# Optimization experiments

Hardware: AMD Instinct MI355X
Metric: run time of the kernel (lower is better)

Reference implementation:

```python
import jax, jax.numpy as jnp
import numpy as np

N = 262144          # number of query points
NUM_AXES = 4        # input_dim + 2
RES = 512           # axis_resolution
EMB = 256           # embedding_dim
OUT = 3             # output_dim
W0 = 30.0           # Sine frequency


def setup_inputs() -> dict:
    key = jax.random.key(0)
    k_c, k_t, k_w1, k_b1, k_w2, k_b2 = jax.random.split(key, 6)
    coords = jax.random.uniform(k_c, (N, 2), jnp.float32, minval=-1.0, maxval=1.0)
    tables = jax.random.normal(k_t, (NUM_AXES, RES, EMB), jnp.float32) * 0.1
    # decoder: Linear(256,256) with first_layer_sine_init, Sine(30), Linear(256,3) with frequency_init(30)
    W1 = jax.random.uniform(k_w1, (256, EMB), jnp.float32, minval=-1.0 / EMB, maxval=1.0 / EMB)
    b1 = jax.random.uniform(k_b1, (256,), jnp.float32, minval=-0.0625, maxval=0.0625)
    lim2 = np.sqrt(6.0 / 256.0) / W0
    W2 = jax.random.uniform(k_w2, (OUT, 256), jnp.float32, minval=-lim2, maxval=lim2)
    b2 = jax.random.uniform(k_b2, (OUT,), jnp.float32, minval=-0.0625, maxval=0.0625)
    return {"coords": coords, "tables": tables, "W1": W1, "b1": b1, "W2": W2, "b2": b2}


def reference(coords, tables, W1, b1, W2, b2):
    # clamp input coords to [-1,1], build the 4 axis coordinates
    c = jnp.clip(coords, -1.0, 1.0)
    c = jnp.concatenate(
        [c, (c[:, 0:1] + c[:, 1:2]) * 0.5, (c[:, 0:1] - c[:, 1:2]) * 0.5], axis=-1
    )  # [N, 4]
    # linearInterpolate (vectorized over all axes at once)
    c = jnp.clip(c, -1.0, 0.999)
    t = (0.5 * c + 0.5) * (tables.shape[1] - 1)       # [N, 4] continuous index
    i0 = jnp.floor(t).astype(jnp.int32)               # [N, 4]
    w = (t - i0)[..., None]                           # [N, 4, 1]
    ax = jnp.arange(tables.shape[0])[None, :]         # [1, 4]
    v0 = tables[ax, i0]                               # [N, 4, EMB] gather
    v1 = tables[ax, i0 + 1]                           # [N, 4, EMB] gather
    emb = jnp.mean((1.0 - w) * v0 + w * v1, axis=1)   # [N, EMB] mean over axes
    # decoder: Linear -> Sine(30) -> Linear
    h = jnp.sin(W0 * (emb @ W1.T + b1))               # [N, 256]
    return h @ W2.T + b2                              # [N, 3]
```

## Files before the change

### kernel.cpp

```cpp
#include <hip/hip_runtime.h>
#include <hip/hip_bf16.h>
#include <hip/hip_fp16.h>

#define NPTS 262144
#define EMB  256
#define RES  512
#define NROWS (4 * RES)

typedef _Float16 half_t;
typedef __attribute__((ext_vector_type(8))) _Float16 half8;

__global__ __launch_bounds__(256) void t2_precompute_kernel(
    const float* __restrict__ tables,
    const float* __restrict__ W1,
    half_t* __restrict__ T2)
{
    __shared__ __align__(16) float arow[8][EMB];
    const int row0 = blockIdx.x * 8;
    const int o = threadIdx.x;

    #pragma unroll
    for (int r = 0; r < 8; ++r)
        arow[r][o] = tables[(row0 + r) * EMB + o];
    __syncthreads();

    float acc[8] = {0.f, 0.f, 0.f, 0.f, 0.f, 0.f, 0.f, 0.f};
    const float4* __restrict__ w1v = reinterpret_cast<const float4*>(W1 + o * EMB);
    for (int ec = 0; ec < EMB / 4; ++ec) {
        const float4 w4 = w1v[ec];
        #pragma unroll
        for (int r = 0; r < 8; ++r) {
            const float4 a4 = *reinterpret_cast<const float4*>(&arow[r][ec * 4]);
            acc[r] = fmaf(w4.x, a4.x, acc[r]);
            acc[r] = fmaf(w4.y, a4.y, acc[r]);
            acc[r] = fmaf(w4.z, a4.z, acc[r]);
            acc[r] = fmaf(w4.w, a4.w, acc[r]);
        }
    }
    const float s = 7.5f * 0.15915494309189535f;
    #pragma unroll
    for (int r = 0; r < 8; ++r)
        T2[(row0 + r) * EMB + o] = (half_t)(s * acc[r]);
}

__global__ __launch_bounds__(256, 8) void eval_kernel(
    const float* __restrict__ coords,
    const half_t* __restrict__ T2,
    const float* __restrict__ b1,
    const float* __restrict__ W2,
    const float* __restrict__ b2,
    float* __restrict__ out)
{
    const int lane = threadIdx.x & 63;
    const int hf   = lane >> 5;
    const int l    = lane & 31;
    const int e0   = l * 8;

    const int wave   = blockIdx.x * 4 + (threadIdx.x >> 6);
    const int nwaves = gridDim.x * 4;

    const float sb = 30.f * 0.15915494309189535f;
    float bias[8];
    float w2r[3][8];
    #pragma unroll
    for (int d = 0; d < 8; ++d) bias[d] = sb * b1[e0 + d];
    #pragma unroll
    for (int j = 0; j < 3; ++j)
        #pragma unroll
        for (int d = 0; d < 8; ++d) w2r[j][d] = W2[j * EMB + e0 + d];
    const float ob0 = b2[0], ob1 = b2[1], ob2 = b2[2];

    const char* __restrict__ T2b = reinterpret_cast<const char*>(T2);

    for (int pp = wave; pp < NPTS / 2; pp += nwaves) {
        const int p = 2 * pp + hf;
        const float2 cf = *reinterpret_cast<const float2*>(coords + 2 * p);
        const float x = fminf(fmaxf(cf.x, -1.f), 1.f);
        const float y = fminf(fmaxf(cf.y, -1.f), 1.f);

        float acc[8];
        #pragma unroll
        for (int d = 0; d < 8; ++d) acc[d] = bias[d];

        #pragma unroll
        for (int a = 0; a < 4; ++a) {
            float c = (a == 0) ? x : (a == 1) ? y
                    : (a == 2) ? 0.5f * (x + y) : 0.5f * (x - y);
            c = fminf(fmaxf(c, -1.f), 0.999f);
            const float t  = fmaf(c, 255.5f, 255.5f);
            const float fi = floorf(t);
            const float w  = t - fi;
            const float omw = 1.f - w;
            const int rowbyte = (((a << 9) + (int)fi) << 9) + (e0 << 1);
            const half8 v0 = *reinterpret_cast<const half8*>(T2b + rowbyte);
            const half8 v1 = *reinterpret_cast<const half8*>(T2b + rowbyte + 512);
            #pragma unroll
            for (int d = 0; d < 8; ++d) {
                acc[d] = fmaf((float)v0[d], omw, acc[d]);
                acc[d] = fmaf((float)v1[d], w,   acc[d]);
            }
        }

        float q0 = 0.f, q1 = 0.f, q2 = 0.f;
        #pragma unroll
        for (int d = 0; d < 8; ++d) {
            const float h = __builtin_amdgcn_sinf(__builtin_amdgcn_fractf(acc[d]));
            q0 = fmaf(h, w2r[0][d], q0);
            q1 = fmaf(h, w2r[1][d], q1);
            q2 = fmaf(h, w2r[2][d], q2);
        }

        #pragma unroll
        for (int off = 16; off > 0; off >>= 1) {
            q0 += __shfl_xor(q0, off, 64);
            q1 += __shfl_xor(q1, off, 64);
            q2 += __shfl_xor(q2, off, 64);
        }

        if (l == 0) {
            out[3 * p + 0] = q0 + ob0;
            out[3 * p + 1] = q1 + ob1;
            out[3 * p + 2] = q2 + ob2;
        }
    }
}

extern "C" void kernel_launch(void* const* d_in, const int* in_sizes, int n_in,
                              void* d_out, int out_size, void* d_ws, size_t ws_size,
                              hipStream_t stream) {
    const float* coords = (const float*)d_in[0];
    const float* tables = (const float*)d_in[1];
    const float* W1     = (const float*)d_in[2];
    const float* b1     = (const float*)d_in[3];
    const float* W2     = (const float*)d_in[4];
    const float* b2     = (const float*)d_in[5];
    float* out = (float*)d_out;

    half_t* T2 = (half_t*)d_ws;

    hipLaunchKernelGGL(t2_precompute_kernel, dim3(NROWS / 8), dim3(256), 0, stream,
                       tables, W1, T2);
    hipLaunchKernelGGL(eval_kernel, dim3(2048), dim3(256), 0, stream,
                       coords, T2, b1, W2, b2, out);
}
```

Before: 68.91 us.

## Use packed fp16 accumulation and 16-lane groups per point in eval kernel

Each wave now handles four points with 16 lanes per point and 16 embedding elements per lane, which shortens the shuffle reduction to four steps. The table interpolation is accumulated in packed half8 arithmetic, so the math can use packed fp16 FMAs instead of converting every element to float. W2 is held in fp16 registers and the occupancy hint in launch_bounds is dropped. The risks are lower precision in the fp16 accumulation of pre-sine arguments, which are scaled by 30/(2π), and higher register pressure.

```diff
diff --git a/kernel.cpp b/kernel.cpp
--- a/kernel.cpp
+++ b/kernel.cpp
@@ -43,7 +43,7 @@
         T2[(row0 + r) * EMB + o] = (half_t)(s * acc[r]);
 }
 
-__global__ __launch_bounds__(256, 8) void eval_kernel(
+__global__ __launch_bounds__(256) void eval_kernel(
     const float* __restrict__ coords,
     const half_t* __restrict__ T2,
     const float* __restrict__ b1,
@@ -52,35 +52,38 @@
     float* __restrict__ out)
 {
     const int lane = threadIdx.x & 63;
-    const int hf   = lane >> 5;
-    const int l    = lane & 31;
-    const int e0   = l * 8;
+    const int g    = lane >> 4;
+    const int l16  = lane & 15;
+    const int e0   = l16 * 16;
 
     const int wave   = blockIdx.x * 4 + (threadIdx.x >> 6);
     const int nwaves = gridDim.x * 4;
 
     const float sb = 30.f * 0.15915494309189535f;
-    float bias[8];
-    float w2r[3][8];
+    float bias[16];
     #pragma unroll
-    for (int d = 0; d < 8; ++d) bias[d] = sb * b1[e0 + d];
+    for (int d = 0; d < 16; ++d) bias[d] = sb * b1[e0 + d];
+
+    half8 w2h[3][2];
     #pragma unroll
     for (int j = 0; j < 3; ++j)
         #pragma unroll
-        for (int d = 0; d < 8; ++d) w2r[j][d] = W2[j * EMB + e0 + d];
+        for (int k = 0; k < 2; ++k)
+            #pragma unroll
+            for (int i = 0; i < 8; ++i)
+                w2h[j][k][i] = (half_t)W2[j * EMB + e0 + k * 8 + i];
+
     const float ob0 = b2[0], ob1 = b2[1], ob2 = b2[2];
-
     const char* __restrict__ T2b = reinterpret_cast<const char*>(T2);
 
-    for (int pp = wave; pp < NPTS / 2; pp += nwaves) {
-        const int p = 2 * pp + hf;
+    for (int pq = wave; pq < NPTS / 4; pq += nwaves) {
+        const int p = 4 * pq + g;
         const float2 cf = *reinterpret_cast<const float2*>(coords + 2 * p);
         const float x = fminf(fmaxf(cf.x, -1.f), 1.f);
         const float y = fminf(fmaxf(cf.y, -1.f), 1.f);
 
-        float acc[8];
-        #pragma unroll
-        for (int d = 0; d < 8; ++d) acc[d] = bias[d];
+        half8 accA = {0, 0, 0, 0, 0, 0, 0, 0};
+        half8 accB = {0, 0, 0, 0, 0, 0, 0, 0};
 
         #pragma unroll
         for (int a = 0; a < 4; ++a) {
@@ -90,34 +93,38 @@
             const float t  = fmaf(c, 255.5f, 255.5f);
             const float fi = floorf(t);
             const float w  = t - fi;
-            const float omw = 1.f - w;
-            const int rowbyte = (((a << 9) + (int)fi) << 9) + (e0 << 1);
-            const half8 v0 = *reinterpret_cast<const half8*>(T2b + rowbyte);
-            const half8 v1 = *reinterpret_cast<const half8*>(T2b + rowbyte + 512);
-            #pragma unroll
-            for (int d = 0; d < 8; ++d) {
-                acc[d] = fmaf((float)v0[d], omw, acc[d]);
-                acc[d] = fmaf((float)v1[d], w,   acc[d]);
-            }
+            const half_t hw   = (half_t)w;
+            const half_t homw = (half_t)(1.f - w);
+            const char* base = T2b + ((((a << 9) + (int)fi) << 9) + (e0 << 1));
+            const half8 v0a = *reinterpret_cast<const half8*>(base);
+            const half8 v0b = *reinterpret_cast<const half8*>(base + 16);
+            const half8 v1a = *reinterpret_cast<const half8*>(base + 512);
+            const half8 v1b = *reinterpret_cast<const half8*>(base + 528);
+            accA = v0a * homw + accA;
+            accA = v1a * hw   + accA;
+            accB = v0b * homw + accB;
+            accB = v1b * hw   + accB;
         }
 
         float q0 = 0.f, q1 = 0.f, q2 = 0.f;
         #pragma unroll
-        for (int d = 0; d < 8; ++d) {
-            const float h = __builtin_amdgcn_sinf(__builtin_amdgcn_fractf(acc[d]));
-            q0 = fmaf(h, w2r[0][d], q0);
-            q1 = fmaf(h, w2r[1][d], q1);
-            q2 = fmaf(h, w2r[2][d], q2);
+        for (int d = 0; d < 16; ++d) {
+            const half_t a16 = (d < 8) ? accA[d] : accB[d - 8];
+            const float arg = fmaf((float)a16, 1.0f, bias[d]);
+            const float h = __builtin_amdgcn_sinf(__builtin_amdgcn_fractf(arg));
+            q0 = fmaf(h, (float)w2h[0][d >> 3][d & 7], q0);
+            q1 = fmaf(h, (float)w2h[1][d >> 3][d & 7], q1);
+            q2 = fmaf(h, (float)w2h[2][d >> 3][d & 7], q2);
         }
 
         #pragma unroll
-        for (int off = 16; off > 0; off >>= 1) {
+        for (int off = 8; off > 0; off >>= 1) {
             q0 += __shfl_xor(q0, off, 64);
             q1 += __shfl_xor(q1, off, 64);
             q2 += __shfl_xor(q2, off, 64);
         }
 
-        if (l == 0) {
+        if (l16 == 0) {
             out[3 * p + 0] = q0 + ob0;
             out[3 * p + 1] = q1 + ob1;
             out[3 * p + 2] = q2 + ob2;
```

Result: faster. 66.36 us (-3.7%).

## Pipeline table gathers across points with packed fp16 interpolation and DPP reduction

Applied to the files above, without the earlier changes.

The eval kernel is restructured so each 16-lane group handles one point and covers 256 dims in two halves. The loop is fully unrolled over 8 points per wave, and the next point's gathers are prefetched while the current one is computed. Interpolation now runs in packed fp16 with half8 FMAs. The output projection uses fdot2, the fract before sin is dropped, and the shuffle reduction becomes a DPP reduction over 16 lanes. This is meant to hide gather latency and cut ALU work, at the cost of fp16 accumulation accuracy, more register pressure (launch bounds drop to 4), and a hardcoded grid-to-point mapping.

```diff
diff --git a/kernel.cpp b/kernel.cpp
--- a/kernel.cpp
+++ b/kernel.cpp
@@ -1,14 +1,13 @@
 #include <hip/hip_runtime.h>
-#include <hip/hip_bf16.h>
 #include <hip/hip_fp16.h>
 
 #define NPTS 262144
 #define EMB  256
-#define RES  512
-#define NROWS (4 * RES)
+#define NROWS 2048
 
 typedef _Float16 half_t;
 typedef __attribute__((ext_vector_type(8))) _Float16 half8;
+typedef __attribute__((ext_vector_type(2))) _Float16 half2v;
 
 __global__ __launch_bounds__(256) void t2_precompute_kernel(
     const float* __restrict__ tables,
@@ -43,7 +42,21 @@
         T2[(row0 + r) * EMB + o] = (half_t)(s * acc[r]);
 }
 
-__global__ __launch_bounds__(256, 8) void eval_kernel(
+template <int CTRL>
+__device__ __forceinline__ float dpp_add(float v) {
+    const int vi = __builtin_bit_cast(int, v);
+    const int sh = __builtin_amdgcn_update_dpp(0, vi, CTRL, 0xF, 0xF, true);
+    return v + __builtin_bit_cast(float, sh);
+}
+__device__ __forceinline__ float reduce16(float v) {
+    v = dpp_add<0xB1>(v);
+    v = dpp_add<0x4E>(v);
+    v = dpp_add<0x141>(v);
+    v = dpp_add<0x140>(v);
+    return v;
+}
+
+__global__ __launch_bounds__(256, 4) void eval_kernel(
     const float* __restrict__ coords,
     const half_t* __restrict__ T2,
     const float* __restrict__ b1,
@@ -52,76 +65,133 @@
     float* __restrict__ out)
 {
     const int lane = threadIdx.x & 63;
-    const int hf   = lane >> 5;
-    const int l    = lane & 31;
-    const int e0   = l * 8;
+    const int g    = lane >> 4;
+    const int l16  = lane & 15;
+    const int dA   = l16 * 8;
+    const int dB   = 128 + l16 * 8;
 
     const int wave   = blockIdx.x * 4 + (threadIdx.x >> 6);
-    const int nwaves = gridDim.x * 4;
+    const int stride = gridDim.x * 4;
 
     const float sb = 30.f * 0.15915494309189535f;
-    float bias[8];
-    float w2r[3][8];
-    #pragma unroll
-    for (int d = 0; d < 8; ++d) bias[d] = sb * b1[e0 + d];
+    half8 biasA, biasB;
+    #pragma unroll
+    for (int i = 0; i < 8; ++i) {
+        biasA[i] = (half_t)(sb * b1[dA + i]);
+        biasB[i] = (half_t)(sb * b1[dB + i]);
+    }
+    half2v w2A[3][4], w2B[3][4];
     #pragma unroll
     for (int j = 0; j < 3; ++j)
         #pragma unroll
-        for (int d = 0; d < 8; ++d) w2r[j][d] = W2[j * EMB + e0 + d];
+        for (int k = 0; k < 4; ++k) {
+            w2A[j][k][0] = (half_t)W2[j * EMB + dA + 2 * k];
+            w2A[j][k][1] = (half_t)W2[j * EMB + dA + 2 * k + 1];
+            w2B[j][k][0] = (half_t)W2[j * EMB + dB + 2 * k];
+            w2B[j][k][1] = (half_t)W2[j * EMB + dB + 2 * k + 1];
+        }
     const float ob0 = b2[0], ob1 = b2[1], ob2 = b2[2];
 
+    int Ca[4];
+    #pragma unroll
+    for (int a = 0; a < 4; ++a) Ca[a] = (a << 18) + (l16 << 4);
+
     const char* __restrict__ T2b = reinterpret_cast<const char*>(T2);
-
-    for (int pp = wave; pp < NPTS / 2; pp += nwaves) {
-        const int p = 2 * pp + hf;
+    const float TMAX = 0.9995f * 511.0f;
+
+    auto calc = [&](int pq, int rb[4], half2v pw[4], int& pOut) {
+        const int p = 4 * pq + g;
+        pOut = p;
         const float2 cf = *reinterpret_cast<const float2*>(coords + 2 * p);
-        const float x = fminf(fmaxf(cf.x, -1.f), 1.f);
-        const float y = fminf(fmaxf(cf.y, -1.f), 1.f);
-
-        float acc[8];
-        #pragma unroll
-        for (int d = 0; d < 8; ++d) acc[d] = bias[d];
-
-        #pragma unroll
-        for (int a = 0; a < 4; ++a) {
-            float c = (a == 0) ? x : (a == 1) ? y
-                    : (a == 2) ? 0.5f * (x + y) : 0.5f * (x - y);
-            c = fminf(fmaxf(c, -1.f), 0.999f);
-            const float t  = fmaf(c, 255.5f, 255.5f);
-            const float fi = floorf(t);
-            const float w  = t - fi;
-            const float omw = 1.f - w;
-            const int rowbyte = (((a << 9) + (int)fi) << 9) + (e0 << 1);
-            const half8 v0 = *reinterpret_cast<const half8*>(T2b + rowbyte);
-            const half8 v1 = *reinterpret_cast<const half8*>(T2b + rowbyte + 512);
-            #pragma unroll
-            for (int d = 0; d < 8; ++d) {
-                acc[d] = fmaf((float)v0[d], omw, acc[d]);
-                acc[d] = fmaf((float)v1[d], w,   acc[d]);
-            }
-        }
+        const float txr = __builtin_amdgcn_fmed3f(fmaf(cf.x, 255.5f, 255.5f), 0.f, 511.f);
+        const float tyr = __builtin_amdgcn_fmed3f(fmaf(cf.y, 255.5f, 255.5f), 0.f, 511.f);
+        float t[4];
+        t[0] = fminf(txr, TMAX);
+        t[1] = fminf(tyr, TMAX);
+        t[2] = fminf((txr + tyr) * 0.5f, TMAX);
+        t[3] = fminf(fmaf(txr - tyr, 0.5f, 255.5f), TMAX);
+        #pragma unroll
+        for (int a = 0; a < 4; ++a) {
+            const int i0 = (int)t[a];
+            const float w = t[a] - (float)i0;
+            rb[a] = (i0 << 9) + Ca[a];
+            pw[a] = __builtin_bit_cast(half2v,
+                        __builtin_amdgcn_cvt_pkrtz(1.f - w, w));
+        }
+    };
+    auto loadA = [&](const int rb[4], half8 A0[4], half8 A1[4]) {
+        #pragma unroll
+        for (int a = 0; a < 4; ++a) {
+            A0[a] = *reinterpret_cast<const half8*>(T2b + rb[a]);
+            A1[a] = *reinterpret_cast<const half8*>(T2b + rb[a] + 512);
+        }
+    };
+    auto loadB = [&](const int rb[4], half8 B0[4], half8 B1[4]) {
+        #pragma unroll
+        for (int a = 0; a < 4; ++a) {
+            B0[a] = *reinterpret_cast<const half8*>(T2b + rb[a] + 256);
+            B1[a] = *reinterpret_cast<const half8*>(T2b + rb[a] + 768);
+        }
+    };
+    auto dots = [&](const half8& acc, const half2v (&w2)[3][4],
+                    float& q0, float& q1, float& q2) {
+        #pragma unroll
+        for (int k = 0; k < 4; ++k) {
+            const float s0 = __builtin_amdgcn_sinf((float)acc[2 * k]);
+            const float s1 = __builtin_amdgcn_sinf((float)acc[2 * k + 1]);
+            const half2v hp = __builtin_bit_cast(half2v,
+                                  __builtin_amdgcn_cvt_pkrtz(s0, s1));
+            q0 = __builtin_amdgcn_fdot2(hp, w2[0][k], q0, false);
+            q1 = __builtin_amdgcn_fdot2(hp, w2[1][k], q1, false);
+            q2 = __builtin_amdgcn_fdot2(hp, w2[2][k], q2, false);
+        }
+    };
+
+    int    rbC[4]; half2v pwC[4]; int pC;
+    int    rbN[4]; half2v pwN[4]; int pN = 0;
+    half8  A0[4], A1[4], B0[4], B1[4];
+
+    calc(wave, rbC, pwC, pC);
+    loadA(rbC, A0, A1);
+    loadB(rbC, B0, B1);
+
+    #pragma unroll
+    for (int k = 0; k < 8; ++k) {
+        if (k < 7) calc(wave + (k + 1) * stride, rbN, pwN, pN);
+
+        half8 accA = biasA;
+        #pragma unroll
+        for (int a = 0; a < 4; ++a) {
+            accA = A0[a] * pwC[a][0] + accA;
+            accA = A1[a] * pwC[a][1] + accA;
+        }
+        if (k < 7) loadA(rbN, A0, A1);
 
         float q0 = 0.f, q1 = 0.f, q2 = 0.f;
-        #pragma unroll
-        for (int d = 0; d < 8; ++d) {
-            const float h = __builtin_amdgcn_sinf(__builtin_amdgcn_fractf(acc[d]));
-            q0 = fmaf(h, w2r[0][d], q0);
-            q1 = fmaf(h, w2r[1][d], q1);
-            q2 = fmaf(h, w2r[2][d], q2);
-        }
-
-        #pragma unroll
-        for (int off = 16; off > 0; off >>= 1) {
-            q0 += __shfl_xor(q0, off, 64);
-            q1 += __shfl_xor(q1, off, 64);
-            q2 += __shfl_xor(q2, off, 64);
-        }
-
-        if (l == 0) {
-            out[3 * p + 0] = q0 + ob0;
-            out[3 * p + 1] = q1 + ob1;
-            out[3 * p + 2] = q2 + ob2;
-        }
+        dots(accA, w2A, q0, q1, q2);
+
+        half8 accB = biasB;
+        #pragma unroll
+        for (int a = 0; a < 4; ++a) {
+            accB = B0[a] * pwC[a][0] + accB;
+            accB = B1[a] * pwC[a][1] + accB;
+        }
+        if (k < 7) loadB(rbN, B0, B1);
+
+        dots(accB, w2B, q0, q1, q2);
+
+        q0 = reduce16(q0);
+        q1 = reduce16(q1);
+        q2 = reduce16(q2);
+
+        if (l16 == 0) {
+            *reinterpret_cast<float3*>(out + 3 * pC) =
+                make_float3(q0 + ob0, q1 + ob1, q2 + ob2);
+        }
+
+        #pragma unroll
+        for (int a = 0; a < 4; ++a) { rbC[a] = rbN[a]; pwC[a] = pwN[a]; }
+        pC = pN;
     }
 }
 
```

New measurement: 55.32 us. 19.7% less time.
